# Kernel optimization log

Hardware: AMD Instinct MI355X
Metric: run time of the kernel (lower is better)

The kernel has to match this reference:

```python
import jax, jax.numpy as jnp
import numpy as np

EMBED_DIM = 128
CANCER_DIM = 32
N_NODES = 50000
N_EDGES = 800000
INPUT_DIM = EMBED_DIM * 2 + CANCER_DIM + 3  # 291
HIDDEN_DIM = INPUT_DIM // 2  # 145


def setup_inputs() -> dict:
    key = jax.random.key(0)
    ks = jax.random.split(key, 8)
    h = jax.random.normal(ks[0], (N_NODES, EMBED_DIM), dtype=jnp.float32)
    edge_index = jax.random.randint(ks[1], (2, N_EDGES), 0, N_NODES, dtype=jnp.int64)
    cancer_embedding = jax.random.normal(ks[2], (1, CANCER_DIM), dtype=jnp.float32)
    causal_scores = jax.random.uniform(ks[3], (N_NODES, 1), dtype=jnp.float32)
    # MLP params (Linear stores weight [out, in]; we keep [in, out] for x @ W)
    lim1 = 1.0 / np.sqrt(INPUT_DIM)
    W1 = jax.random.uniform(ks[4], (INPUT_DIM, HIDDEN_DIM), minval=-lim1, maxval=lim1, dtype=jnp.float32)
    b1 = jax.random.uniform(ks[5], (HIDDEN_DIM,), minval=-lim1, maxval=lim1, dtype=jnp.float32)
    lim2 = 1.0 / np.sqrt(HIDDEN_DIM)
    W2 = jax.random.uniform(ks[6], (HIDDEN_DIM, 1), minval=-lim2, maxval=lim2, dtype=jnp.float32)
    b2 = jax.random.uniform(ks[7], (1,), minval=-lim2, maxval=lim2, dtype=jnp.float32)
    return {"h": h, "edge_index": edge_index, "cancer_embedding": cancer_embedding,
            "causal_scores": causal_scores, "W1": W1, "b1": b1, "W2": W2, "b2": b2}


def reference(h, edge_index, cancer_embedding, causal_scores, W1, b1, W2, b2):
    src, dst = edge_index[0], edge_index[1]
    h_i = h[src]                         # [E, D]
    h_j = h[dst]                         # [E, D]
    c_i = causal_scores[src]             # [E, 1]
    c_j = causal_scores[dst]             # [E, 1]
    causal_diff = c_i - c_j              # [E, 1]
    num_edges = edge_index.shape[1]
    cancer_exp = jnp.broadcast_to(cancer_embedding, (num_edges, cancer_embedding.shape[-1]))
    edge_features = jnp.concatenate([h_i, h_j, cancer_exp, c_i, c_j, causal_diff], axis=-1)  # [E, INPUT_DIM]
    hid = jax.nn.relu(edge_features @ W1 + b1)          # [E, HIDDEN]
    out = jax.nn.sigmoid(hid @ W2 + b2)                 # [E, 1]
    return out.squeeze(-1)                              # [E]
```

## Files before the change

kernel.cpp:

```cpp
#include <hip/hip_runtime.h>
#include <hip/hip_bf16.h>
#include <stdint.h>

#define EMBED 128
#define HID 145
#define HSTR 160
#define NTILE 20
#define KCH 4
#define MROWB 128
#define LROW 152
#define HS4ROW 33

typedef __attribute__((ext_vector_type(8))) short short8;
typedef __attribute__((ext_vector_type(4))) float f32x4;

__device__ __forceinline__ uint16_t f2bf(float f) {
    uint32_t x = __float_as_uint(f);
    x += 0x7FFFu + ((x >> 16) & 1u);
    return (uint16_t)(x >> 16);
}
__device__ __forceinline__ short f2bf_cvt(float f) {
    union { __bf16 h; short s; } u_;
    u_.h = (__bf16)f;
    return u_.s;
}

__global__ void __launch_bounds__(256)
prep_fused(const float* __restrict__ cancer, const float* __restrict__ W1,
           const float* __restrict__ b1, const float* __restrict__ W2,
           const void* __restrict__ eiv, int E, int P,
           float* __restrict__ b1p, float* __restrict__ wci,
           float* __restrict__ wcj, float* __restrict__ w2p,
           short* __restrict__ Wpb, uint32_t* __restrict__ pairs)
{
    const int t = threadIdx.x;
    const int b = blockIdx.x;
    if (b < P) {
        const uint32_t* pw = (const uint32_t*)eiv;
        const uint32_t odd = pw[1] | pw[3] | pw[5] | pw[7] | pw[9] | pw[11] | pw[13] | pw[15];
        const int is64 = (odd == 0u);
        const int e = b * 256 + t;
        if (e < E) {
            uint32_t src, dst;
            if (is64) {
                const long long* e64 = (const long long*)eiv;
                src = (uint32_t)e64[e]; dst = (uint32_t)e64[(size_t)E + e];
            } else {
                const uint32_t* e32 = (const uint32_t*)eiv;
                src = e32[e];           dst = e32[(size_t)E + e];
            }
            pairs[e] = (src << 16) | (dst & 0xFFFFu);
        }
        return;
    }
    if (b < P + 160) {
        const int idx = (b - P) * 256 + t;
        const int reg  = idx & 7;
        const int lane = (idx >> 3) & 63;
        const int tl   = idx >> 9;
        const int tt   = tl % NTILE;
        const int kc   = tl / NTILE;
        const int k    = kc * 32 + (lane >> 4) * 8 + reg;
        const int col  = tt * 16 + (lane & 15);
        float val = 0.f;
        if (col < HID)                             val = W1[(size_t)k * HID + col];
        else if (col >= HSTR && col < HSTR + HID)  val = W1[(size_t)(EMBED + k) * HID + (col - HSTR)];
        Wpb[idx] = (short)f2bf(val);
        return;
    }
    if (t < HSTR) {
        float bv = 0.f, a = 0.f, bb = 0.f, w2 = 0.f;
        if (t < HID) {
            float s = b1[t];
            #pragma unroll
            for (int k = 0; k < 32; ++k)
                s = fmaf(cancer[k], W1[(size_t)(2 * EMBED + k) * HID + t], s);
            bv = s;
            a  = W1[(size_t)288 * HID + t] + W1[(size_t)290 * HID + t];
            bb = W1[(size_t)289 * HID + t] - W1[(size_t)290 * HID + t];
            w2 = W2[t];
        }
        b1p[t] = bv; wci[t] = a; wcj[t] = bb; w2p[t] = w2;
    }
}

__global__ void __launch_bounds__(256)
proj_mfma(const float* __restrict__ h, const short* __restrict__ Wpb,
          const float* __restrict__ causal, const float* __restrict__ b1p,
          const float* __restrict__ wci, const float* __restrict__ wcj,
          uint8_t* __restrict__ u, uint8_t* __restrict__ v, int nNodes)
{
    __shared__ __align__(16) uint8_t smem[64 * HS4ROW * 16];
    float4* hs4 = (float4*)smem;

    const int t = threadIdx.x;
    const int lane = t & 63;
    const int w = t >> 6;
    const int lane15 = lane & 15, hi = lane >> 4;
    const int n0blk = blockIdx.x * 64;
    const int nbase = n0blk + w * 16;

    const float4* hsrc = (const float4*)(h + (size_t)n0blk * EMBED);
    if (n0blk + 64 <= nNodes) {
        #pragma unroll
        for (int k = 0; k < 8; ++k) {
            const int f = k * 256 + t;
            hs4[(f >> 5) * HS4ROW + (f & 31)] = hsrc[f];
        }
    } else {
        #pragma unroll
        for (int k = 0; k < 8; ++k) {
            const int f = k * 256 + t;
            const int row = f >> 5;
            float4 val = make_float4(0.f, 0.f, 0.f, 0.f);
            if (n0blk + row < nNodes) val = hsrc[f];
            hs4[row * HS4ROW + (f & 31)] = val;
        }
    }
    __syncthreads();

    const float4* hrow4 = hs4 + (w * 16 + lane15) * HS4ROW + hi * 2;
    short8 afr[KCH];
    #pragma unroll
    for (int kc = 0; kc < KCH; ++kc) {
        const float4 x = hrow4[kc * 8];
        const float4 y = hrow4[kc * 8 + 1];
        short8 a;
        a[0] = f2bf_cvt(x.x); a[1] = f2bf_cvt(x.y);
        a[2] = f2bf_cvt(x.z); a[3] = f2bf_cvt(x.w);
        a[4] = f2bf_cvt(y.x); a[5] = f2bf_cvt(y.y);
        a[6] = f2bf_cvt(y.z); a[7] = f2bf_cvt(y.w);
        afr[kc] = a;
    }

    f32x4 acc[NTILE];
    #pragma unroll
    for (int tt = 0; tt < NTILE; ++tt) acc[tt] = (f32x4){0.f, 0.f, 0.f, 0.f};

    const short8* bp = (const short8*)Wpb;
    #pragma unroll
    for (int kc = 0; kc < KCH; ++kc) {
        #pragma unroll
        for (int tt = 0; tt < NTILE; ++tt) {
            const short8 b = bp[(kc * NTILE + tt) * 64 + lane];
            acc[tt] = __builtin_amdgcn_mfma_f32_16x16x32_bf16(afr[kc], b, acc[tt], 0, 0, 0);
        }
    }

    float cz[4];
    #pragma unroll
    for (int j = 0; j < 4; ++j) {
        const int n = nbase + hi * 4 + j;
        cz[j] = (n < nNodes) ? causal[n] : 0.f;
    }

    #pragma unroll
    for (int tt = 0; tt < NTILE; ++tt) {
        const int col = tt * 16 + lane15;
        const bool isU = (tt < 10);
        const int ccol = isU ? col : col - HSTR;
        const float addB = isU ? b1p[ccol] : 0.f;
        const float addC = isU ? wci[ccol] : wcj[ccol];
        #pragma unroll
        for (int j = 0; j < 4; ++j)
            acc[tt][j] = acc[tt][j] + fmaf(cz[j], addC, addB);
    }

    __syncthreads();

    uint8_t* ldsu = smem;
    uint8_t* ldsv = smem + 64 * LROW;

    #pragma unroll
    for (int j = 0; j < 4; ++j) {
        float mu = fmaxf(fmaxf(fmaxf(fabsf(acc[0][j]), fabsf(acc[1][j])),
                               fmaxf(fabsf(acc[2][j]), fabsf(acc[3][j]))),
                         fmaxf(fmaxf(fabsf(acc[4][j]), fabsf(acc[5][j])),
                               fmaxf(fmaxf(fabsf(acc[6][j]), fabsf(acc[7][j])),
                                     fmaxf(fabsf(acc[8][j]), fabsf(acc[9][j])))));
        float mv = fmaxf(fmaxf(fmaxf(fabsf(acc[10][j]), fabsf(acc[11][j])),
                               fmaxf(fabsf(acc[12][j]), fabsf(acc[13][j]))),
                         fmaxf(fmaxf(fabsf(acc[14][j]), fabsf(acc[15][j])),
                               fmaxf(fmaxf(fabsf(acc[16][j]), fabsf(acc[17][j])),
                                     fmaxf(fabsf(acc[18][j]), fabsf(acc[19][j])))));
        #pragma unroll
        for (int m = 1; m < 16; m <<= 1) {
            mu = fmaxf(mu, __shfl_xor(mu, m));
            mv = fmaxf(mv, __shfl_xor(mv, m));
        }
        mu = fmaxf(mu, 1e-20f); mv = fmaxf(mv, 1e-20f);
        const float invu = 31.f / mu, su = mu * (1.f / 31.f);
        const float invv = 31.f / mv, sv = mv * (1.f / 31.f);
        const int row = w * 16 + hi * 4 + j;
        uint8_t* lu = ldsu + row * LROW + lane15;
        uint8_t* lv = ldsv + row * LROW + lane15;
        #pragma unroll
        for (int tt = 0; tt < 9; ++tt) {
            lu[16 * tt] = (uint8_t)(uint32_t)(acc[tt][j]      * invu + 32.5f);
            lv[16 * tt] = (uint8_t)(uint32_t)(acc[10 + tt][j] * invv + 32.5f);
        }
        if (lane15 == 0) {
            lu[144] = (uint8_t)(uint32_t)(acc[9][j]  * invu + 32.5f);
            lv[144] = (uint8_t)(uint32_t)(acc[19][j] * invv + 32.5f);
            *(float*)(ldsu + row * LROW + 148) = su;
            *(float*)(ldsv + row * LROW + 148) = sv;
        }
    }
    __syncthreads();

    char* ug = (char*)u + (size_t)n0blk * MROWB;
    char* vg = (char*)v + (size_t)n0blk * MROWB;
    const bool full = (n0blk + 64 <= nNodes);
    #pragma unroll
    for (int i = 0; i < 2; ++i) {
        const int idx = i * 256 + t;
        const int row = idx >> 3, c = idx & 7;
        if (!full && n0blk + row >= nNodes) continue;
        #pragma unroll
        for (int tab = 0; tab < 2; ++tab) {
            const uint8_t* lr = (tab ? ldsv : ldsu) + row * LROW;
            uint4 o;
            if (c < 7) {
                const uint32_t* wp = (const uint32_t*)(lr + 20 * c);
                const uint32_t b0 = wp[0], b1_ = wp[1], b2 = wp[2], b3 = wp[3], b4 = wp[4];
                o.x = (b0 & 63u) | (((b0 >> 8) & 63u) << 6) | (((b0 >> 16) & 63u) << 12)
                    | (((b0 >> 24) & 63u) << 18) | ((b1_ & 63u) << 24);
                o.y = ((b1_ >> 8) & 63u) | (((b1_ >> 16) & 63u) << 6) | (((b1_ >> 24) & 63u) << 12)
                    | ((b2 & 63u) << 18) | (((b2 >> 8) & 63u) << 24);
                o.z = ((b2 >> 16) & 63u) | (((b2 >> 24) & 63u) << 6) | ((b3 & 63u) << 12)
                    | (((b3 >> 8) & 63u) << 18) | (((b3 >> 16) & 63u) << 24);
                o.w = ((b3 >> 24) & 63u) | ((b4 & 63u) << 6) | (((b4 >> 8) & 63u) << 12)
                    | (((b4 >> 16) & 63u) << 18) | (((b4 >> 24) & 63u) << 24);
            } else {
                const uint32_t w0 = *(const uint32_t*)(lr + 140);
                const uint32_t w1 = *(const uint32_t*)(lr + 144);
                o.x = (w0 & 63u) | (((w0 >> 8) & 63u) << 6) | (((w0 >> 16) & 63u) << 12)
                    | (((w0 >> 24) & 63u) << 18) | ((w1 & 63u) << 24);
                o.y = *(const uint32_t*)(lr + 148);
                o.z = 0u; o.w = 0u;
            }
            *(uint4*)((tab ? vg : ug) + 16 * idx) = o;
        }
    }
}

__global__ void __launch_bounds__(256)
edge_int6(const uint32_t* __restrict__ pairs,
          const uint8_t* __restrict__ u, const uint8_t* __restrict__ v,
          const float* __restrict__ w2p, const float* __restrict__ b2,
          float* __restrict__ out, int E)
{
    const int t = threadIdx.x;
    const int lane = t & 63;
    const int r = lane & 3;
    const int grp = lane >> 2;
    const int wid = blockIdx.x * (blockDim.x >> 6) + (t >> 6);
    const int base = wid * 32;
    const int e0 = base + grp, e1 = base + 16 + grp;
    const bool ok0 = e0 < E, ok1 = e1 < E;
    const float bias2 = *b2;

    const uint32_t pr0 = pairs[ok0 ? e0 : 0];
    const uint32_t pr1 = pairs[ok1 ? e1 : 0];

    const uint4* ua = (const uint4*)(u + (pr0 >> 16)     * (uint32_t)MROWB) + 2 * r;
    const uint4* va = (const uint4*)(v + (pr0 & 0xFFFFu) * (uint32_t)MROWB) + 2 * r;
    const uint4* ub = (const uint4*)(u + (pr1 >> 16)     * (uint32_t)MROWB) + 2 * r;
    const uint4* vb = (const uint4*)(v + (pr1 & 0xFFFFu) * (uint32_t)MROWB) + 2 * r;
    const uint4 UA0 = ua[0], UA1 = ua[1];
    const uint4 VA0 = va[0], VA1 = va[1];
    const uint4 UB0 = ub[0], UB1 = ub[1];
    const uint4 VB0 = vb[0], VB1 = vb[1];

    const int l3 = lane | 3;
    const float su0 = __shfl(__uint_as_float(UA1.y), l3);
    const float sv0 = __shfl(__uint_as_float(VA1.y), l3);
    const float su1 = __shfl(__uint_as_float(UB1.y), l3);
    const float sv1 = __shfl(__uint_as_float(VB1.y), l3);
    const float off0 = -32.f * (su0 + sv0);
    const float off1 = -32.f * (su1 + sv1);

    uint32_t uw0[8] = {UA0.x, UA0.y, UA0.z, UA0.w, UA1.x, UA1.y, UA1.z, UA1.w};
    uint32_t vw0[8] = {VA0.x, VA0.y, VA0.z, VA0.w, VA1.x, VA1.y, VA1.z, VA1.w};
    uint32_t uw1[8] = {UB0.x, UB0.y, UB0.z, UB0.w, UB1.x, UB1.y, UB1.z, UB1.w};
    uint32_t vw1[8] = {VB0.x, VB0.y, VB0.z, VB0.w, VB1.x, VB1.y, VB1.z, VB1.w};

    const float* w2b = w2p + 40 * r;
    float acc0 = 0.f, acc1 = 0.f;
    #pragma unroll
    for (int lw = 0; lw < 8; ++lw) {
        #pragma unroll
        for (int k = 0; k < 5; ++k) {
            const float w2v = w2b[5 * lw + k];
            const float uf0 = (float)((uw0[lw] >> (6 * k)) & 63u);
            const float vf0 = (float)((vw0[lw] >> (6 * k)) & 63u);
            float tv0 = fmaf(su0, uf0, fmaf(sv0, vf0, off0));
            tv0 = fmaxf(tv0, 0.f);
            acc0 = fmaf(tv0, w2v, acc0);
            const float uf1 = (float)((uw1[lw] >> (6 * k)) & 63u);
            const float vf1 = (float)((vw1[lw] >> (6 * k)) & 63u);
            float tv1 = fmaf(su1, uf1, fmaf(sv1, vf1, off1));
            tv1 = fmaxf(tv1, 0.f);
            acc1 = fmaf(tv1, w2v, acc1);
        }
    }
    acc0 += __shfl_xor(acc0, 1);
    acc0 += __shfl_xor(acc0, 2);
    acc1 += __shfl_xor(acc1, 1);
    acc1 += __shfl_xor(acc1, 2);
    if (r == 0 && ok0) out[e0] = 1.f / (1.f + __expf(-(acc0 + bias2)));
    if (r == 0 && ok1) out[e1] = 1.f / (1.f + __expf(-(acc1 + bias2)));
}

__global__ void __launch_bounds__(256)
fallback_kernel(const void* __restrict__ eiv, const float* __restrict__ h,
                const float* __restrict__ cancer, const float* __restrict__ causal,
                const float* __restrict__ W1, const float* __restrict__ b1,
                const float* __restrict__ W2, const float* __restrict__ b2,
                float* __restrict__ out, int E)
{
    const int lane = threadIdx.x & 63;
    const int wpb  = blockDim.x >> 6;
    const int wid  = blockIdx.x * wpb + (threadIdx.x >> 6);
    const int nW   = gridDim.x * wpb;
    const uint32_t* p32 = (const uint32_t*)eiv;
    const uint32_t o = p32[1] | p32[3] | p32[5] | p32[7] | p32[9] | p32[11] | p32[13] | p32[15];
    const int is64 = (o == 0u);
    const long long* e64 = (const long long*)eiv;
    const int*       e32 = (const int*)eiv;
    const float bias2 = *b2;

    for (int e = wid; e < E; e += nW) {
        long long src, dst;
        if (is64) { src = e64[e]; dst = e64[(size_t)E + e]; }
        else      { src = e32[e]; dst = e32[(size_t)E + e]; }
        const float ci = causal[src], cj = causal[dst];
        float acc0 = 0.f, acc1 = 0.f, acc2 = 0.f;
        const int j0 = lane, j1 = lane + 64, j2 = lane + 128;
        for (int k = 0; k < 291; ++k) {
            float f;
            if      (k < 128) f = h[(size_t)src * 128 + k];
            else if (k < 256) f = h[(size_t)dst * 128 + (k - 128)];
            else if (k < 288) f = cancer[k - 256];
            else if (k == 288) f = ci;
            else if (k == 289) f = cj;
            else               f = ci - cj;
            const float* wr = W1 + (size_t)k * HID;
            acc0 = fmaf(f, wr[j0], acc0);
            acc1 = fmaf(f, wr[j1], acc1);
            if (j2 < HID) acc2 = fmaf(f, wr[j2], acc2);
        }
        float partial = fmaxf(acc0 + b1[j0], 0.f) * W2[j0]
                      + fmaxf(acc1 + b1[j1], 0.f) * W2[j1];
        if (j2 < HID) partial += fmaxf(acc2 + b1[j2], 0.f) * W2[j2];
        #pragma unroll
        for (int m = 32; m; m >>= 1) partial += __shfl_xor(partial, m, 64);
        if (lane == 0) out[e] = 1.f / (1.f + __expf(-(partial + bias2)));
    }
}

extern "C" void kernel_launch(void* const* d_in, const int* in_sizes, int n_in,
                              void* d_out, int out_size, void* d_ws, size_t ws_size,
                              hipStream_t stream)
{
    const float* h      = (const float*)d_in[0];
    const void*  ei     = d_in[1];
    const float* cancer = (const float*)d_in[2];
    const float* causal = (const float*)d_in[3];
    const float* W1     = (const float*)d_in[4];
    const float* b1     = (const float*)d_in[5];
    const float* W2     = (const float*)d_in[6];
    const float* b2     = (const float*)d_in[7];
    float* outp = (float*)d_out;

    const int nNodes = in_sizes[0] / EMBED;
    const int E      = in_sizes[1] / 2;

    const size_t WPB_OFF   = 8192;
    const size_t PAIRS_OFF = 98304;
    const size_t pairsB    = ((size_t)E * 4 + 255) & ~(size_t)255;
    const size_t tabB      = (size_t)nNodes * MROWB;
    const size_t U_OFF     = PAIRS_OFF + pairsB;
    const size_t V_OFF     = (U_OFF + tabB + 255) & ~(size_t)255;
    const size_t need      = V_OFF + tabB;

    char* ws = (char*)d_ws;
    float* b1p  = (float*)(ws + 1024);
    float* wci  = (float*)(ws + 2048);
    float* wcj  = (float*)(ws + 3072);
    float* w2p  = (float*)(ws + 4096);
    short* Wpb  = (short*)(ws + WPB_OFF);

    if (ws_size >= need && nNodes <= 65536) {
        uint32_t* pairs = (uint32_t*)(ws + PAIRS_OFF);
        uint8_t*  u     = (uint8_t*)(ws + U_OFF);
        uint8_t*  v     = (uint8_t*)(ws + V_OFF);

        const int P = (E + 255) / 256;
        prep_fused<<<P + 161, 256, 0, stream>>>(cancer, W1, b1, W2, ei, E, P,
                                                b1p, wci, wcj, w2p, Wpb, pairs);
        proj_mfma<<<(nNodes + 63) / 64, 256, 0, stream>>>(h, Wpb, causal, b1p,
                                                          wci, wcj, u, v, nNodes);
        const int waves  = (E + 31) / 32;
        const int blocks = (waves + 3) / 4;
        edge_int6<<<blocks, 256, 0, stream>>>(pairs, u, v, w2p, b2, outp, E);
    } else {
        fallback_kernel<<<2048, 256, 0, stream>>>(ei, h, cancer, causal, W1, b1, W2, b2,
                                                  outp, E);
    }
}
```

Before: 81.15 us.

## Split projection MFMA work by output-column tiles across waves, store h as bf16 in LDS

The node-projection kernel now converts h to bf16 once while staging it into shared memory, and each wave computes 5 column tiles for all 64 rows instead of all 20 tiles for its own 16 rows. Each wave therefore loads only a quarter of the packed weight fragments per block, which cuts global/L2 weight traffic, and the smaller LDS footprint may raise occupancy. Because a row's values are now spread across two waves, the per-row absmax for 6-bit quantization is combined through a small shared pmax array with an extra barrier. A guard drops padded columns at 145 and above.

```diff
diff --git a/kernel.cpp b/kernel.cpp
--- a/kernel.cpp
+++ b/kernel.cpp
@@ -9,7 +9,7 @@
 #define KCH 4
 #define MROWB 128
 #define LROW 152
-#define HS4ROW 33
+#define HB2ROW 272
 
 typedef __attribute__((ext_vector_type(8))) short short8;
 typedef __attribute__((ext_vector_type(4))) float f32x4;
@@ -90,127 +90,132 @@
           const float* __restrict__ wci, const float* __restrict__ wcj,
           uint8_t* __restrict__ u, uint8_t* __restrict__ v, int nNodes)
 {
-    __shared__ __align__(16) uint8_t smem[64 * HS4ROW * 16];
-    float4* hs4 = (float4*)smem;
+    __shared__ __align__(16) uint8_t smem[2 * 64 * LROW];
+    __shared__ float pmax[2][2][64];
 
     const int t = threadIdx.x;
     const int lane = t & 63;
     const int w = t >> 6;
     const int lane15 = lane & 15, hi = lane >> 4;
     const int n0blk = blockIdx.x * 64;
-    const int nbase = n0blk + w * 16;
+    const bool full = (n0blk + 64 <= nNodes);
 
     const float4* hsrc = (const float4*)(h + (size_t)n0blk * EMBED);
-    if (n0blk + 64 <= nNodes) {
+    if (full) {
         #pragma unroll
         for (int k = 0; k < 8; ++k) {
             const int f = k * 256 + t;
-            hs4[(f >> 5) * HS4ROW + (f & 31)] = hsrc[f];
+            const float4 x = hsrc[f];
+            const uint32_t lo = (uint32_t)(uint16_t)f2bf_cvt(x.x)
+                              | ((uint32_t)(uint16_t)f2bf_cvt(x.y) << 16);
+            const uint32_t hg = (uint32_t)(uint16_t)f2bf_cvt(x.z)
+                              | ((uint32_t)(uint16_t)f2bf_cvt(x.w) << 16);
+            *(uint2*)(smem + (f >> 5) * HB2ROW + (f & 31) * 8) = make_uint2(lo, hg);
         }
     } else {
         #pragma unroll
         for (int k = 0; k < 8; ++k) {
             const int f = k * 256 + t;
             const int row = f >> 5;
-            float4 val = make_float4(0.f, 0.f, 0.f, 0.f);
-            if (n0blk + row < nNodes) val = hsrc[f];
-            hs4[row * HS4ROW + (f & 31)] = val;
+            float4 x = make_float4(0.f, 0.f, 0.f, 0.f);
+            if (n0blk + row < nNodes) x = hsrc[f];
+            const uint32_t lo = (uint32_t)(uint16_t)f2bf_cvt(x.x)
+                              | ((uint32_t)(uint16_t)f2bf_cvt(x.y) << 16);
+            const uint32_t hg = (uint32_t)(uint16_t)f2bf_cvt(x.z)
+                              | ((uint32_t)(uint16_t)f2bf_cvt(x.w) << 16);
+            *(uint2*)(smem + row * HB2ROW + (f & 31) * 8) = make_uint2(lo, hg);
         }
     }
     __syncthreads();
 
-    const float4* hrow4 = hs4 + (w * 16 + lane15) * HS4ROW + hi * 2;
-    short8 afr[KCH];
+    const int w5 = 5 * w;
+    const uint8_t* habase = smem + lane15 * HB2ROW + hi * 16;
+
+    f32x4 acc[4][5];
+    #pragma unroll
+    for (int g = 0; g < 4; ++g)
+        #pragma unroll
+        for (int i = 0; i < 5; ++i) acc[g][i] = (f32x4){0.f, 0.f, 0.f, 0.f};
+
+    const short8* bp = (const short8*)Wpb;
     #pragma unroll
     for (int kc = 0; kc < KCH; ++kc) {
-        const float4 x = hrow4[kc * 8];
-        const float4 y = hrow4[kc * 8 + 1];
-        short8 a;
-        a[0] = f2bf_cvt(x.x); a[1] = f2bf_cvt(x.y);
-        a[2] = f2bf_cvt(x.z); a[3] = f2bf_cvt(x.w);
-        a[4] = f2bf_cvt(y.x); a[5] = f2bf_cvt(y.y);
-        a[6] = f2bf_cvt(y.z); a[7] = f2bf_cvt(y.w);
-        afr[kc] = a;
-    }
-
-    f32x4 acc[NTILE];
-    #pragma unroll
-    for (int tt = 0; tt < NTILE; ++tt) acc[tt] = (f32x4){0.f, 0.f, 0.f, 0.f};
-
-    const short8* bp = (const short8*)Wpb;
-    #pragma unroll
-    for (int kc = 0; kc < KCH; ++kc) {
-        #pragma unroll
-        for (int tt = 0; tt < NTILE; ++tt) {
-            const short8 b = bp[(kc * NTILE + tt) * 64 + lane];
-            acc[tt] = __builtin_amdgcn_mfma_f32_16x16x32_bf16(afr[kc], b, acc[tt], 0, 0, 0);
-        }
-    }
-
-    float cz[4];
-    #pragma unroll
-    for (int j = 0; j < 4; ++j) {
-        const int n = nbase + hi * 4 + j;
-        cz[j] = (n < nNodes) ? causal[n] : 0.f;
-    }
-
-    #pragma unroll
-    for (int tt = 0; tt < NTILE; ++tt) {
-        const int col = tt * 16 + lane15;
-        const bool isU = (tt < 10);
-        const int ccol = isU ? col : col - HSTR;
-        const float addB = isU ? b1p[ccol] : 0.f;
-        const float addC = isU ? wci[ccol] : wcj[ccol];
-        #pragma unroll
-        for (int j = 0; j < 4; ++j)
-            acc[tt][j] = acc[tt][j] + fmaf(cz[j], addC, addB);
-    }
-
+        short8 bfr[5];
+        #pragma unroll
+        for (int i = 0; i < 5; ++i)
+            bfr[i] = bp[(kc * NTILE + w5 + i) * 64 + lane];
+        #pragma unroll
+        for (int g = 0; g < 4; ++g) {
+            const short8 a = *(const short8*)(habase + g * 16 * HB2ROW + kc * 64);
+            #pragma unroll
+            for (int i = 0; i < 5; ++i)
+                acc[g][i] = __builtin_amdgcn_mfma_f32_16x16x32_bf16(a, bfr[i], acc[g][i], 0, 0, 0);
+        }
+    }
+
+    const int tb = w >> 1, hf = w & 1;
+    float addB[5], addC[5];
+    #pragma unroll
+    for (int i = 0; i < 5; ++i) {
+        const int col = (w5 + i) * 16 + lane15;
+        const int ccol = tb ? col - HSTR : col;
+        addB[i] = tb ? 0.f : b1p[ccol];
+        addC[i] = tb ? wcj[ccol] : wci[ccol];
+    }
+    #pragma unroll
+    for (int g = 0; g < 4; ++g) {
+        float cz[4];
+        #pragma unroll
+        for (int j = 0; j < 4; ++j) {
+            const int n = n0blk + g * 16 + hi * 4 + j;
+            cz[j] = (n < nNodes) ? causal[n] : 0.f;
+        }
+        #pragma unroll
+        for (int i = 0; i < 5; ++i)
+            #pragma unroll
+            for (int j = 0; j < 4; ++j)
+                acc[g][i][j] += fmaf(cz[j], addC[i], addB[i]);
+    }
+
+    #pragma unroll
+    for (int g = 0; g < 4; ++g) {
+        #pragma unroll
+        for (int j = 0; j < 4; ++j) {
+            float m = fmaxf(fmaxf(fmaxf(fabsf(acc[g][0][j]), fabsf(acc[g][1][j])),
+                                  fmaxf(fabsf(acc[g][2][j]), fabsf(acc[g][3][j]))),
+                            fabsf(acc[g][4][j]));
+            #pragma unroll
+            for (int mk = 1; mk < 16; mk <<= 1) m = fmaxf(m, __shfl_xor(m, mk));
+            if (lane15 == 0) pmax[tb][hf][g * 16 + hi * 4 + j] = m;
+        }
+    }
     __syncthreads();
 
     uint8_t* ldsu = smem;
     uint8_t* ldsv = smem + 64 * LROW;
-
-    #pragma unroll
-    for (int j = 0; j < 4; ++j) {
-        float mu = fmaxf(fmaxf(fmaxf(fabsf(acc[0][j]), fabsf(acc[1][j])),
-                               fmaxf(fabsf(acc[2][j]), fabsf(acc[3][j]))),
-                         fmaxf(fmaxf(fabsf(acc[4][j]), fabsf(acc[5][j])),
-                               fmaxf(fmaxf(fabsf(acc[6][j]), fabsf(acc[7][j])),
-                                     fmaxf(fabsf(acc[8][j]), fabsf(acc[9][j])))));
-        float mv = fmaxf(fmaxf(fmaxf(fabsf(acc[10][j]), fabsf(acc[11][j])),
-                               fmaxf(fabsf(acc[12][j]), fabsf(acc[13][j]))),
-                         fmaxf(fmaxf(fabsf(acc[14][j]), fabsf(acc[15][j])),
-                               fmaxf(fmaxf(fabsf(acc[16][j]), fabsf(acc[17][j])),
-                                     fmaxf(fabsf(acc[18][j]), fabsf(acc[19][j])))));
-        #pragma unroll
-        for (int m = 1; m < 16; m <<= 1) {
-            mu = fmaxf(mu, __shfl_xor(mu, m));
-            mv = fmaxf(mv, __shfl_xor(mv, m));
-        }
-        mu = fmaxf(mu, 1e-20f); mv = fmaxf(mv, 1e-20f);
-        const float invu = 31.f / mu, su = mu * (1.f / 31.f);
-        const float invv = 31.f / mv, sv = mv * (1.f / 31.f);
-        const int row = w * 16 + hi * 4 + j;
-        uint8_t* lu = ldsu + row * LROW + lane15;
-        uint8_t* lv = ldsv + row * LROW + lane15;
-        #pragma unroll
-        for (int tt = 0; tt < 9; ++tt) {
-            lu[16 * tt] = (uint8_t)(uint32_t)(acc[tt][j]      * invu + 32.5f);
-            lv[16 * tt] = (uint8_t)(uint32_t)(acc[10 + tt][j] * invv + 32.5f);
-        }
-        if (lane15 == 0) {
-            lu[144] = (uint8_t)(uint32_t)(acc[9][j]  * invu + 32.5f);
-            lv[144] = (uint8_t)(uint32_t)(acc[19][j] * invv + 32.5f);
-            *(float*)(ldsu + row * LROW + 148) = su;
-            *(float*)(ldsv + row * LROW + 148) = sv;
+    uint8_t* myt = tb ? ldsv : ldsu;
+    #pragma unroll
+    for (int g = 0; g < 4; ++g) {
+        #pragma unroll
+        for (int j = 0; j < 4; ++j) {
+            const int row = g * 16 + hi * 4 + j;
+            const float mm = fmaxf(fmaxf(pmax[tb][0][row], pmax[tb][1][row]), 1e-20f);
+            const float inv = 31.f / mm;
+            if (hf == 0 && lane15 == 0)
+                *(float*)(myt + row * LROW + 148) = mm * (1.f / 31.f);
+            #pragma unroll
+            for (int i = 0; i < 5; ++i) {
+                const int ccol = (w5 + i) * 16 + lane15 - (tb ? HSTR : 0);
+                const uint8_t q = (uint8_t)(uint32_t)(acc[g][i][j] * inv + 32.5f);
+                if (ccol < 145)
+                    myt[row * LROW + ccol] = q;
+            }
         }
     }
     __syncthreads();
 
     char* ug = (char*)u + (size_t)n0blk * MROWB;
     char* vg = (char*)v + (size_t)n0blk * MROWB;
-    const bool full = (n0blk + 64 <= nNodes);
     #pragma unroll
     for (int i = 0; i < 2; ++i) {
         const int idx = i * 256 + t;
```

Result: faster. 66.59 us (-17.9%).
